# Performance work log

Measured on AMD Instinct MI355X. Metric: run time of the kernel, lower is better.

Reference implementation:

```python
import jax, jax.numpy as jnp
import numpy as np

EPS = 1e-8
N, E = 30000, 480000
SI, VI, SE, VE = 128, 16, 32, 1


def _norm_no_nan(x, axis=-1, keepdims=False, eps=EPS, sqrt=True):
    out = jnp.maximum(jnp.sum(x * x, axis=axis, keepdims=keepdims), eps)
    return jnp.sqrt(out) if sqrt else out


def _gvp(s, v, wh, wsw, wsb, wv, act):
    # v: [n, vi, 3]; wh: [h, vi]; wsw: [so, si+h]; wv: [vo, h]
    vh = jnp.einsum('nct,hc->nht', v, wh)                 # [n, h, 3]
    vn = _norm_no_nan(vh, axis=-1)                        # [n, h]
    s_out = jnp.concatenate([s, vn], -1) @ wsw.T + wsb    # [n, so]
    v_out = jnp.einsum('nht,oh->not', vh, wv)             # [n, vo, 3]
    if act:
        v_out = v_out * jax.nn.sigmoid(_norm_no_nan(v_out, axis=-1, keepdims=True))
        s_out = jax.nn.relu(s_out)
    return s_out, v_out


def _layernorm(s, v, g, b):
    mu = jnp.mean(s, -1, keepdims=True)
    var = jnp.mean((s - mu) ** 2, -1, keepdims=True)
    s = (s - mu) / jnp.sqrt(var + 1e-5) * g + b
    vn = jnp.maximum(jnp.sum(v * v, -1, keepdims=True), EPS)          # [n, vc, 1] squared norms
    mask = (vn > 2 * EPS).astype(v.dtype)
    vm = jnp.sum(vn * mask, -2, keepdims=True) / (EPS + jnp.sum(mask, -2, keepdims=True))
    vm = jnp.sqrt(vm + EPS)
    v = mask * (v / vm)
    return s, v


def setup_inputs() -> dict:
    key = jax.random.key(0)
    ks = iter(jax.random.split(key, 40))

    def p(shape):
        return (jax.random.normal(next(ks), shape, jnp.float32) / np.float32(np.sqrt(shape[-1])))

    inp = {
        's': jax.random.normal(next(ks), (N, SI), jnp.float32),
        'v': jax.random.normal(next(ks), (N, VI, 3), jnp.float32),
        'edge_index': jax.random.randint(next(ks), (2, E), 0, N),
        'edge_s': jax.random.normal(next(ks), (E, SE), jnp.float32),
        'edge_v': jax.random.normal(next(ks), (E, VE, 3), jnp.float32),
    }
    smi, vmi = 2 * SI + SE, 2 * VI + VE      # 288, 33
    h1 = max(vmi, VI)                        # 33
    # message GVP 1: (288,33)->(128,16)
    inp['m1_wh'], inp['m1_wsw'], inp['m1_wsb'], inp['m1_wv'] = p((h1, vmi)), p((SI, smi + h1)), jnp.zeros((SI,), jnp.float32), p((VI, h1))
    # message GVP 2/3: (128,16)->(128,16), h=16
    inp['m2_wh'], inp['m2_wsw'], inp['m2_wsb'], inp['m2_wv'] = p((VI, VI)), p((SI, SI + VI)), jnp.zeros((SI,), jnp.float32), p((VI, VI))
    inp['m3_wh'], inp['m3_wsw'], inp['m3_wsb'], inp['m3_wv'] = p((VI, VI)), p((SI, SI + VI)), jnp.zeros((SI,), jnp.float32), p((VI, VI))
    # feedforward: (128,16)->(512,32)->(128,16)
    sh, vh = 4 * SI, 2 * VI                  # 512, 32
    inp['f1_wh'], inp['f1_wsw'], inp['f1_wsb'], inp['f1_wv'] = p((vh, VI)), p((sh, SI + vh)), jnp.zeros((sh,), jnp.float32), p((vh, vh))
    inp['f2_wh'], inp['f2_wsw'], inp['f2_wsb'], inp['f2_wv'] = p((vh, vh)), p((SI, sh + vh)), jnp.zeros((SI,), jnp.float32), p((VI, vh))
    inp['ln0_g'], inp['ln0_b'] = jnp.ones((SI,), jnp.float32), jnp.zeros((SI,), jnp.float32)
    inp['ln1_g'], inp['ln1_b'] = jnp.ones((SI,), jnp.float32), jnp.zeros((SI,), jnp.float32)
    return inp


def reference(s, v, edge_index, edge_s, edge_v,
              m1_wh, m1_wsw, m1_wsb, m1_wv,
              m2_wh, m2_wsw, m2_wsb, m2_wv,
              m3_wh, m3_wsw, m3_wsb, m3_wv,
              f1_wh, f1_wsw, f1_wsb, f1_wv,
              f2_wh, f2_wsw, f2_wsb, f2_wv,
              ln0_g, ln0_b, ln1_g, ln1_b):
    src, dst = edge_index[0], edge_index[1]
    # gather: tuple_cat((s_j, v_j), edge_attr, (s_i, v_i))
    ms = jnp.concatenate([s[src], edge_s, s[dst]], -1)           # [E, 288]
    mv = jnp.concatenate([v[src], edge_v, v[dst]], -2)           # [E, 33, 3]
    ms, mv = _gvp(ms, mv, m1_wh, m1_wsw, m1_wsb, m1_wv, act=True)
    ms, mv = _gvp(ms, mv, m2_wh, m2_wsw, m2_wsb, m2_wv, act=True)
    ms, mv = _gvp(ms, mv, m3_wh, m3_wsw, m3_wsb, m3_wv, act=False)
    # scatter-mean aggregate to destination nodes
    cnt = jnp.maximum(jax.ops.segment_sum(jnp.ones((mv.shape[0],), ms.dtype), dst, N), 1.0)
    agg_s = jax.ops.segment_sum(ms, dst, N) / cnt[:, None]
    agg_v = jax.ops.segment_sum(mv, dst, N) / cnt[:, None, None]
    # residual + norm (dropout is identity at eval)
    s1, v1 = _layernorm(s + agg_s, v + agg_v, ln0_g, ln0_b)
    # feedforward
    fs, fv = _gvp(s1, v1, f1_wh, f1_wsw, f1_wsb, f1_wv, act=True)
    fs, fv = _gvp(fs, fv, f2_wh, f2_wsw, f2_wsb, f2_wv, act=False)
    s2, v2 = _layernorm(s1 + fs, v1 + fv, ln1_g, ln1_b)
    return s2, v2
```

## Files before the change

kernel.cpp:

```cpp
#include <hip/hip_runtime.h>

#define EPSF 1e-8f

typedef __attribute__((ext_vector_type(8))) short short8;
typedef __attribute__((ext_vector_type(4))) short short4v;
typedef __attribute__((ext_vector_type(4))) float float4v;

__device__ __forceinline__ unsigned bfhi_bits(float x) {
    unsigned u = __float_as_uint(x);
    return (u + 0x7fffu + ((u >> 16) & 1u)) >> 16;
}
__device__ __forceinline__ float bits2f(unsigned b) { return __uint_as_float(b << 16); }
__device__ __forceinline__ void split_bf(float x, unsigned short& h, unsigned short& l) {
    unsigned hb = bfhi_bits(x);
    h = (unsigned short)hb;
    l = (unsigned short)bfhi_bits(x - bits2f(hb));
}

template<int NH>
__device__ __forceinline__ void matvec3_v(const float* __restrict__ wrow,
                                          const float* prow,
                                          float& a0, float& a1, float& a2)
{
    #pragma unroll
    for (int g = 0; g < NH / 4; ++g) {
        const float4 f0 = ((const float4*)prow)[3 * g + 0];
        const float4 f1 = ((const float4*)prow)[3 * g + 1];
        const float4 f2 = ((const float4*)prow)[3 * g + 2];
        const float w0 = wrow[4 * g + 0], w1 = wrow[4 * g + 1];
        const float w2 = wrow[4 * g + 2], w3 = wrow[4 * g + 3];
        a0 = fmaf(w0, f0.x, a0); a1 = fmaf(w0, f0.y, a1); a2 = fmaf(w0, f0.z, a2);
        a0 = fmaf(w1, f0.w, a0); a1 = fmaf(w1, f1.x, a1); a2 = fmaf(w1, f1.y, a2);
        a0 = fmaf(w2, f1.z, a0); a1 = fmaf(w2, f1.w, a1); a2 = fmaf(w2, f2.x, a2);
        a0 = fmaf(w3, f2.y, a0); a1 = fmaf(w3, f2.z, a1); a2 = fmaf(w3, f2.w, a2);
    }
}

__global__ void pack_w(const float* __restrict__ W, unsigned short* __restrict__ hi,
                       unsigned short* __restrict__ lo, int NO, int K, int steps) {
    const int gid = blockIdx.x * 256 + threadIdx.x;
    const int total = (NO >> 4) * steps * 512;
    if (gid >= total) return;
    const int j = gid & 7, l = (gid >> 3) & 63, rest = gid >> 9;
    const int t = rest % steps, nt = rest / steps;
    const int n = nt * 16 + (l & 15);
    const int k = t * 32 + ((l >> 4) << 3) + j;
    const float x = (k < K) ? W[(size_t)n * K + k] : 0.f;
    unsigned short h, lw;
    split_bf(x, h, lw);
    hi[gid] = h; lo[gid] = lw;
}

__global__ void pack_m1e(const float* __restrict__ W, unsigned short* __restrict__ hi,
                         unsigned short* __restrict__ lo) {
    const int gid = blockIdx.x * 256 + threadIdx.x;
    if (gid >= 12288) return;
    const int j = gid & 7, l = (gid >> 3) & 63, rest = gid >> 9;
    const int t = rest % 3, nt = rest / 3;
    const int n = nt * 16 + (l & 15);
    const int k = t * 32 + ((l >> 4) << 3) + j;
    float x = 0.f;
    if (k < 32)      x = W[(size_t)n * 321 + 128 + k];
    else if (k < 65) x = W[(size_t)n * 321 + 288 + (k - 32)];
    unsigned short h, lw; split_bf(x, h, lw);
    hi[gid] = h; lo[gid] = lw;
}

__global__ void pack_m1n(const float* __restrict__ W, unsigned short* __restrict__ hi,
                         unsigned short* __restrict__ lo) {
    const int gid = blockIdx.x * 256 + threadIdx.x;
    if (gid >= 32768) return;
    const int j = gid & 7, l = (gid >> 3) & 63, rest = gid >> 9;
    const int t = rest & 3, nt = rest >> 2;
    const int n = nt * 16 + (l & 15);
    const int k = t * 32 + ((l >> 4) << 3) + j;
    const float x = (n < 128) ? W[(size_t)n * 321 + k]
                              : W[(size_t)(n - 128) * 321 + 160 + k];
    unsigned short h, lw; split_bf(x, h, lw);
    hi[gid] = h; lo[gid] = lw;
}

template<int STEPS, int NTPW, int ASTR, int MCLAMP = 15>
__device__ __forceinline__ void kloop(const unsigned short* PAh, const unsigned short* PAl,
    const unsigned short* __restrict__ wph, const unsigned short* __restrict__ wpl,
    float4v* acc, int lane, int wave)
{
    const int m = (lane & 15) & MCLAMP, q = lane >> 4;
    for (int t = 0; t < STEPS; ++t) {
        const int k0 = t * 32 + q * 8;
        const short8 ah = *(const short8*)(PAh + m * ASTR + k0);
        const short8 al = *(const short8*)(PAl + m * ASTR + k0);
        #pragma unroll
        for (int i = 0; i < NTPW; ++i) {
            const int nt = wave * NTPW + i;
            const size_t off = ((size_t)(nt * STEPS + t) * 64 + lane) * 8;
            const short8 bh = *(const short8*)(wph + off);
            const short8 bl = *(const short8*)(wpl + off);
            acc[i] = __builtin_amdgcn_mfma_f32_16x16x32_bf16(ah, bh, acc[i], 0, 0, 0);
            acc[i] = __builtin_amdgcn_mfma_f32_16x16x32_bf16(al, bh, acc[i], 0, 0, 0);
            acc[i] = __builtin_amdgcn_mfma_f32_16x16x32_bf16(ah, bl, acc[i], 0, 0, 0);
        }
    }
}

constexpr int PAS = 136;

__global__ __launch_bounds__(256)
void node_pre(const float* __restrict__ s, const float* __restrict__ v,
              const float* __restrict__ m1_wh, const float* __restrict__ m1_wsb,
              const unsigned short* __restrict__ pnh, const unsigned short* __restrict__ pnl,
              float* __restrict__ Pg, float* __restrict__ Q1g, float* __restrict__ Q3g,
              int N)
{
    __shared__ __align__(16) unsigned short Ah[16 * PAS], Al[16 * PAS];
    __shared__ __align__(16) float Vs[16 * 48];

    const int tid = threadIdx.x, lane = tid & 63, wave = tid >> 6;
    const int e = tid & 15, q16 = tid >> 4;
    const int n0 = blockIdx.x * 16;
    const int ne = min(n0 + e, N - 1);

    {
        const float* sp = s + (size_t)ne * 128 + q16 * 8;
        const float4 x = ((const float4*)sp)[0];
        const float4 y = ((const float4*)sp)[1];
        short8 hv, lv; unsigned short h, l;
        split_bf(x.x, h, l); hv[0] = h; lv[0] = l;
        split_bf(x.y, h, l); hv[1] = h; lv[1] = l;
        split_bf(x.z, h, l); hv[2] = h; lv[2] = l;
        split_bf(x.w, h, l); hv[3] = h; lv[3] = l;
        split_bf(y.x, h, l); hv[4] = h; lv[4] = l;
        split_bf(y.y, h, l); hv[5] = h; lv[5] = l;
        split_bf(y.z, h, l); hv[6] = h; lv[6] = l;
        split_bf(y.w, h, l); hv[7] = h; lv[7] = l;
        *(short8*)(Ah + e * PAS + q16 * 8) = hv;
        *(short8*)(Al + e * PAS + q16 * 8) = lv;
    }
    if (q16 < 12)
        ((float4*)(Vs + e * 48))[q16] = ((const float4*)(v + (size_t)ne * 48))[q16];
    __syncthreads();

    {
        float4v acc[4] = {{0,0,0,0},{0,0,0,0},{0,0,0,0},{0,0,0,0}};
        kloop<4, 4, PAS>(Ah, Al, pnh, pnl, acc, lane, wave);
        const int q = lane >> 4;
        #pragma unroll
        for (int i = 0; i < 4; ++i) {
            const int j = (wave * 4 + i) * 16 + (lane & 15);
            const float bias = (j < 128) ? m1_wsb[j] : 0.f;
            #pragma unroll
            for (int r = 0; r < 4; ++r) {
                const int m = q * 4 + r;
                if (n0 + m < N) Pg[(size_t)(n0 + m) * 256 + j] = acc[i][r] + bias;
            }
        }
    }
    #pragma unroll
    for (int k = 0; k < 7; ++k) {
        const int idx = tid + k * 256;
        if (idx < 16 * 99) {
            const int n = idx & 15, j = idx >> 4;
            const int h = j / 3, t = j - h * 3;
            const float* vb = Vs + n * 48 + t;
            const float* w = m1_wh + h * 33;
            float a1 = 0.f, a3 = 0.f;
            for (int c = 0; c < 16; ++c) {
                const float vv = vb[c * 3];
                a1 = fmaf(w[c], vv, a1);
                a3 = fmaf(w[17 + c], vv, a3);
            }
            const int nn = n0 + n;
            if (nn < N) {
                Q1g[(size_t)nn * 100 + j] = a1;
                Q3g[(size_t)nn * 100 + j] = a3;
            }
        }
    }
}

constexpr int SA2 = 168;
constexpr int SBs = 168;
constexpr int SB1 = 100;
constexpr int SB2 = 52;
constexpr int SPS = 132;

__global__ __launch_bounds__(256)
void edge_kernel(const int* __restrict__ eidx,
                 const float* __restrict__ es, const float* __restrict__ ev,
                 const float* __restrict__ m1_wh, const float* __restrict__ m1_wv,
                 const float* __restrict__ m2_wh, const float* __restrict__ m2_wsb,
                 const float* __restrict__ m2_wv,
                 const float* __restrict__ m3_wh, const float* __restrict__ m3_wsb,
                 const float* __restrict__ m3_wv,
                 const unsigned short* __restrict__ p1h, const unsigned short* __restrict__ p1l,
                 const unsigned short* __restrict__ p2h, const unsigned short* __restrict__ p2l,
                 const unsigned short* __restrict__ p3h, const unsigned short* __restrict__ p3l,
                 const float* __restrict__ Pg, const float* __restrict__ Q1g,
                 const float* __restrict__ Q3g,
                 double* __restrict__ agg_s, double* __restrict__ agg_v,
                 float* __restrict__ cnt, int E)
{
    __shared__ __align__(16) unsigned short Ah[16 * SA2], Al[16 * SA2];
    __shared__ __align__(16) float SP[16 * SPS];
    __shared__ __align__(16) float B1[16 * SB1];
    __shared__ int ssrc[16], sgd[16], sdst[16], seid[16];

    unsigned short* PBh = Ah;
    unsigned short* PBl = Al;
    float* B2 = SP;

    const int tid = threadIdx.x, lane = tid & 63, wave = tid >> 6;
    const int e = tid & 15, q16 = tid >> 4;
    const int e0 = blockIdx.x * 16;

    const int eg_r = e0 + e;
    const int ee_r = (eg_r < E) ? eg_r : (E - 1);
    const int src_r = eidx[ee_r];
    const int dst_r = eidx[E + ee_r];

    if (q16 < 8) {
        const float4 x = ((const float4*)(es + (size_t)ee_r * 32))[q16];
        short4v hv, lv; unsigned short h, l;
        split_bf(x.x, h, l); hv[0] = h; lv[0] = l;
        split_bf(x.y, h, l); hv[1] = h; lv[1] = l;
        split_bf(x.z, h, l); hv[2] = h; lv[2] = l;
        split_bf(x.w, h, l); hv[3] = h; lv[3] = l;
        *(short4v*)(Ah + e * SA2 + 4 * q16) = hv;
        *(short4v*)(Al + e * SA2 + 4 * q16) = lv;
    }
    { const int c = 65 + q16; Ah[e * SA2 + c] = 0; Al[e * SA2 + c] = 0; }
    { const int c = 81 + q16; if (c < 96) { Ah[e * SA2 + c] = 0; Al[e * SA2 + c] = 0; } }
    {
        const float* P1 = Pg + (size_t)src_r * 256;
        const float* P3 = Pg + (size_t)dst_r * 256 + 128;
        const float4 a0 = ((const float4*)P1)[2 * q16];
        const float4 a1 = ((const float4*)P1)[2 * q16 + 1];
        const float4 b0 = ((const float4*)P3)[2 * q16];
        const float4 b1 = ((const float4*)P3)[2 * q16 + 1];
        float4 r0, r1;
        r0.x = a0.x + b0.x; r0.y = a0.y + b0.y; r0.z = a0.z + b0.z; r0.w = a0.w + b0.w;
        r1.x = a1.x + b1.x; r1.y = a1.y + b1.y; r1.z = a1.z + b1.z; r1.w = a1.w + b1.w;
        float4* o = (float4*)(SP + e * SPS + 8 * q16);
        o[0] = r0; o[1] = r1;
    }
    if (tid < 16) {
        const int eg = e0 + tid;
        const bool ok = (eg < E);
        const int ee = ok ? eg : (E - 1);
        seid[tid] = ee;
        ssrc[tid] = eidx[ee];
        const int d = eidx[E + ee];
        sgd[tid] = d;
        sdst[tid] = ok ? d : -1;
    }
    __syncthreads();

    #pragma unroll
    for (int k = 0; k < 3; ++k) {
        const int idx = tid + k * 256;
        if (idx < 528) {
            const int h = idx >> 4, e2 = idx & 15;
            const float* q1 = Q1g + (size_t)ssrc[e2] * 100 + h * 3;
            const float* q3 = Q3g + (size_t)sgd[e2] * 100 + h * 3;
            const float* evp = ev + (size_t)seid[e2] * 3;
            const float w16 = m1_wh[h * 33 + 16];
            const float v0 = q1[0] + q3[0] + w16 * evp[0];
            const float v1 = q1[1] + q3[1] + w16 * evp[1];
            const float v2 = q1[2] + q3[2] + w16 * evp[2];
            float* o = B1 + e2 * SB1 + h * 3;
            o[0] = v0; o[1] = v1; o[2] = v2;
            const float vn = sqrtf(fmaxf(v0 * v0 + v1 * v1 + v2 * v2, EPSF));
            unsigned short hh, ll; split_bf(vn, hh, ll);
            Ah[e2 * SA2 + 32 + h] = hh; Al[e2 * SA2 + 32 + h] = ll;
        }
    }
    __syncthreads();

    float4v acc1[2] = {{0,0,0,0},{0,0,0,0}};
    kloop<3, 2, SA2>(Ah, Al, p1h, p1l, acc1, lane, wave);
    __syncthreads();

    {
        const int q = lane >> 4;
        #pragma unroll
        for (int i = 0; i < 2; ++i) {
            const int n = (wave * 2 + i) * 16 + (lane & 15);
            #pragma unroll
            for (int r = 0; r < 4; ++r) {
                const int m = q * 4 + r;
                const float x = fmaxf(acc1[i][r] + SP[m * SPS + n], 0.f);
                unsigned short h, l; split_bf(x, h, l);
                PBh[m * SBs + n] = h; PBl[m * SBs + n] = l;
            }
        }
    }
    __syncthreads();

    {
        const int o = q16;
        const float* wrow = m1_wv + o * 33;
        const float* prow = B1 + e * SB1;
        float a0 = 0.f, a1 = 0.f, a2 = 0.f;
        matvec3_v<32>(wrow, prow, a0, a1, a2);
        const float w32 = wrow[32];
        a0 = fmaf(w32, prow[96], a0); a1 = fmaf(w32, prow[97], a1); a2 = fmaf(w32, prow[98], a2);
        const float nrm = sqrtf(fmaxf(a0 * a0 + a1 * a1 + a2 * a2, EPSF));
        const float sg = 1.f / (1.f + __expf(-nrm));
        float* p2 = B2 + e * SB2 + o * 3;
        p2[0] = a0 * sg; p2[1] = a1 * sg; p2[2] = a2 * sg;
    }
    __syncthreads();

    {
        const int h = q16;
        float a0 = 0.f, a1 = 0.f, a2 = 0.f;
        matvec3_v<16>(m2_wh + h * 16, B2 + e * SB2, a0, a1, a2);
        float* o = B1 + e * SB1 + h * 3;
        o[0] = a0; o[1] = a1; o[2] = a2;
        const float vn = sqrtf(fmaxf(a0 * a0 + a1 * a1 + a2 * a2, EPSF));
        unsigned short hh, ll; split_bf(vn, hh, ll);
        PBh[e * SBs + 128 + h] = hh; PBl[e * SBs + 128 + h] = ll;
        PBh[e * SBs + 144 + h] = 0;  PBl[e * SBs + 144 + h] = 0;
    }
    __syncthreads();

    float4v acc2[2] = {{0,0,0,0},{0,0,0,0}};
    kloop<5, 2, SBs>(PBh, PBl, p2h, p2l, acc2, lane, wave);
    __syncthreads();

    {
        const int q = lane >> 4;
        #pragma unroll
        for (int i = 0; i < 2; ++i) {
            const int n = (wave * 2 + i) * 16 + (lane & 15);
            const float bias = m2_wsb[n];
            #pragma unroll
            for (int r = 0; r < 4; ++r) {
                const int m = q * 4 + r;
                const float x = fmaxf(acc2[i][r] + bias, 0.f);
                unsigned short h, l; split_bf(x, h, l);
                Ah[m * SA2 + n] = h; Al[m * SA2 + n] = l;
            }
        }
    }
    {
        const int o = q16;
        float a0 = 0.f, a1 = 0.f, a2 = 0.f;
        matvec3_v<16>(m2_wv + o * 16, B1 + e * SB1, a0, a1, a2);
        const float nrm = sqrtf(fmaxf(a0 * a0 + a1 * a1 + a2 * a2, EPSF));
        const float sg = 1.f / (1.f + __expf(-nrm));
        float* p2 = B2 + e * SB2 + o * 3;
        p2[0] = a0 * sg; p2[1] = a1 * sg; p2[2] = a2 * sg;
    }
    __syncthreads();

    {
        const int h = q16;
        float a0 = 0.f, a1 = 0.f, a2 = 0.f;
        matvec3_v<16>(m3_wh + h * 16, B2 + e * SB2, a0, a1, a2);
        float* o = B1 + e * SB1 + h * 3;
        o[0] = a0; o[1] = a1; o[2] = a2;
        const float vn = sqrtf(fmaxf(a0 * a0 + a1 * a1 + a2 * a2, EPSF));
        unsigned short hh, ll; split_bf(vn, hh, ll);
        Ah[e * SA2 + 128 + h] = hh; Al[e * SA2 + 128 + h] = ll;
        Ah[e * SA2 + 144 + h] = 0;  Al[e * SA2 + 144 + h] = 0;
    }
    __syncthreads();

    float4v acc3[2] = {{0,0,0,0},{0,0,0,0}};
    kloop<5, 2, SA2>(Ah, Al, p3h, p3l, acc3, lane, wave);
    {
        const int o = q16;
        float a0 = 0.f, a1 = 0.f, a2 = 0.f;
        matvec3_v<16>(m3_wv + o * 16, B1 + e * SB1, a0, a1, a2);
        float* p2 = B2 + e * SB2 + o * 3;
        p2[0] = a0; p2[1] = a1; p2[2] = a2;
    }
    __syncthreads();

    {
        const int q = lane >> 4;
        #pragma unroll
        for (int i = 0; i < 2; ++i) {
            const int n = (wave * 2 + i) * 16 + (lane & 15);
            const float bias = m3_wsb[n];
            #pragma unroll
            for (int r = 0; r < 4; ++r) {
                const int m = q * 4 + r;
                const int d = sdst[m];
                if (d >= 0) atomicAdd(&agg_s[(size_t)d * 128 + n], (double)(acc3[i][r] + bias));
            }
        }
    }
    #pragma unroll
    for (int it = 0; it < 3; ++it) {
        const int j = q16 + 16 * it;
        const int d = sdst[e];
        if (d >= 0) atomicAdd(&agg_v[(size_t)d * 48 + j], (double)B2[e * SB2 + j]);
    }
    if (tid < 16 && sdst[tid] >= 0) atomicAdd(&cnt[sdst[tid]], 1.0f);
}

template<int NE, int SSTR, int VSTR>
__device__ __forceinline__ void layer_normT(float* S, float* V,
    const float* __restrict__ g, const float* __restrict__ b, float* red, int lane)
{
    #pragma unroll
    for (int e = 0; e < NE; ++e) {
        float x0 = S[e * SSTR + lane], x1 = S[e * SSTR + 64 + lane];
        float sum = x0 + x1;
        #pragma unroll
        for (int off = 32; off > 0; off >>= 1) sum += __shfl_xor(sum, off, 64);
        const float mu = sum * (1.f / 128.f);
        const float d0 = x0 - mu, d1 = x1 - mu;
        float vs = d0 * d0 + d1 * d1;
        #pragma unroll
        for (int off = 32; off > 0; off >>= 1) vs += __shfl_xor(vs, off, 64);
        const float rstd = rsqrtf(vs * (1.f / 128.f) + 1e-5f);
        S[e * SSTR + lane]      = d0 * rstd * g[lane]      + b[lane];
        S[e * SSTR + 64 + lane] = d1 * rstd * g[lane + 64] + b[lane + 64];

        if (lane < 16) {
            const float a = V[e * VSTR + lane * 3], bb = V[e * VSTR + lane * 3 + 1],
                        cc = V[e * VSTR + lane * 3 + 2];
            const float vn = fmaxf(a * a + bb * bb + cc * cc, EPSF);
            red[lane]      = vn;
            red[16 + lane] = (vn > 2.f * EPSF) ? 1.f : 0.f;
        }
        __syncthreads();
        float sn = 0.f, sm = 0.f;
        #pragma unroll
        for (int i = 0; i < 16; ++i) { sn += red[i] * red[16 + i]; sm += red[16 + i]; }
        const float rvm = rsqrtf(sn / (EPSF + sm) + EPSF);
        if (lane < 48) V[e * VSTR + lane] = red[16 + lane / 3] * V[e * VSTR + lane] * rvm;
        __syncthreads();
    }
}

constexpr int NNS  = 132;
constexpr int NNV  = 52;
constexpr int NNH  = 100;
constexpr int NA1n = 168;
constexpr int NA2n = 552;

__global__ __launch_bounds__(128)
void node_kernel(const float* __restrict__ s, const float* __restrict__ v,
                 const float* __restrict__ f1_wh, const float* __restrict__ f1_wsb,
                 const float* __restrict__ f1_wv,
                 const float* __restrict__ f2_wh, const float* __restrict__ f2_wsb,
                 const float* __restrict__ f2_wv,
                 const float* __restrict__ ln0_g, const float* __restrict__ ln0_b,
                 const float* __restrict__ ln1_g, const float* __restrict__ ln1_b,
                 const unsigned short* __restrict__ pf1h, const unsigned short* __restrict__ pf1l,
                 const unsigned short* __restrict__ pf2h, const unsigned short* __restrict__ pf2l,
                 const double* __restrict__ agg_s, const double* __restrict__ agg_v,
                 const float* __restrict__ cnt,
                 float* __restrict__ out, int N)
{
    __shared__ __align__(16) unsigned short UBh[8 * NA1n], UBl[8 * NA1n];
    __shared__ __align__(16) unsigned short UB2h[8 * NA2n], UB2l[8 * NA2n];
    __shared__ __align__(16) float S1f[8 * NNS];
    __shared__ __align__(16) float V1f[8 * NNV];
    __shared__ __align__(16) float VH[8 * NNH];
    __shared__ __align__(16) float FV[8 * NNH];
    __shared__ float red[2 * 32];

    const int tid = threadIdx.x, lane = tid & 63, wave = tid >> 6;
    const int e = tid & 7, qq = tid >> 3;
    const int n0 = blockIdx.x * 8;

    bool oks[4];
    #pragma unroll
    for (int e4 = 0; e4 < 4; ++e4) {
        const int idx = wave * 4 + e4;
        const int ng = n0 + idx;
        oks[e4] = (ng < N);
        const int n = oks[e4] ? ng : (N - 1);
        const double inv = 1.0 / (double)fmaxf(cnt[n], 1.f);
        if (lane < 32) {
            const float4 a = ((const float4*)(s + (size_t)n * 128))[lane];
            const double2 b0 = ((const double2*)(agg_s + (size_t)n * 128))[2 * lane];
            const double2 b1 = ((const double2*)(agg_s + (size_t)n * 128))[2 * lane + 1];
            float4 r;
            r.x = (float)((double)a.x + b0.x * inv);
            r.y = (float)((double)a.y + b0.y * inv);
            r.z = (float)((double)a.z + b1.x * inv);
            r.w = (float)((double)a.w + b1.y * inv);
            ((float4*)(S1f + idx * NNS))[lane] = r;
        }
        if (lane < 12) {
            const float4 a = ((const float4*)(v + (size_t)n * 48))[lane];
            const double2 b0 = ((const double2*)(agg_v + (size_t)n * 48))[2 * lane];
            const double2 b1 = ((const double2*)(agg_v + (size_t)n * 48))[2 * lane + 1];
            float4 r;
            r.x = (float)((double)a.x + b0.x * inv);
            r.y = (float)((double)a.y + b0.y * inv);
            r.z = (float)((double)a.z + b1.x * inv);
            r.w = (float)((double)a.w + b1.y * inv);
            ((float4*)(V1f + idx * NNV))[lane] = r;
        }
    }
    __syncthreads();

    layer_normT<4, NNS, NNV>(S1f + wave * 4 * NNS, V1f + wave * 4 * NNV,
                             ln0_g, ln0_b, red + wave * 32, lane);

    {
        const float* sp = S1f + e * NNS + qq * 8;
        short8 hv, lv; unsigned short h, l;
        #pragma unroll
        for (int j = 0; j < 8; ++j) { split_bf(sp[j], h, l); hv[j] = h; lv[j] = l; }
        *(short8*)(UBh + e * NA1n + qq * 8) = hv;
        *(short8*)(UBl + e * NA1n + qq * 8) = lv;
    }
    #pragma unroll
    for (int hi = 0; hi < 2; ++hi) {
        const int h = qq + 16 * hi;
        float a0 = 0.f, a1 = 0.f, a2 = 0.f;
        matvec3_v<16>(f1_wh + h * 16, V1f + e * NNV, a0, a1, a2);
        float* o = VH + e * NNH + h * 3;
        o[0] = a0; o[1] = a1; o[2] = a2;
        const float vn = sqrtf(fmaxf(a0 * a0 + a1 * a1 + a2 * a2, EPSF));
        unsigned short hh, ll; split_bf(vn, hh, ll);
        UBh[e * NA1n + 128 + h] = hh; UBl[e * NA1n + 128 + h] = ll;
    }
    __syncthreads();

    {
        float4v acc1[16];
        #pragma unroll
        for (int i = 0; i < 16; ++i) acc1[i] = (float4v){0.f, 0.f, 0.f, 0.f};
        kloop<5, 16, NA1n>(UBh, UBl, pf1h, pf1l, acc1, lane, wave);
        const int q = lane >> 4;
        #pragma unroll
        for (int i = 0; i < 16; ++i) {
            const int n = (wave * 16 + i) * 16 + (lane & 15);
            const float bias = f1_wsb[n];
            #pragma unroll
            for (int r = 0; r < 4; ++r) {
                const int m = q * 4 + r;
                if (m < 8) {
                    const float x = fmaxf(acc1[i][r] + bias, 0.f);
                    unsigned short h, l; split_bf(x, h, l);
                    UB2h[m * NA2n + n] = h; UB2l[m * NA2n + n] = l;
                }
            }
        }
    }
    #pragma unroll
    for (int oi = 0; oi < 2; ++oi) {
        const int o = qq + 16 * oi;
        float a0 = 0.f, a1 = 0.f, a2 = 0.f;
        matvec3_v<32>(f1_wv + o * 32, VH + e * NNH, a0, a1, a2);
        const float nrm = sqrtf(fmaxf(a0 * a0 + a1 * a1 + a2 * a2, EPSF));
        const float sg = 1.f / (1.f + __expf(-nrm));
        float* p2 = FV + e * NNH + o * 3;
        p2[0] = a0 * sg; p2[1] = a1 * sg; p2[2] = a2 * sg;
    }
    __syncthreads();

    #pragma unroll
    for (int hi = 0; hi < 2; ++hi) {
        const int h = qq + 16 * hi;
        float a0 = 0.f, a1 = 0.f, a2 = 0.f;
        matvec3_v<32>(f2_wh + h * 32, FV + e * NNH, a0, a1, a2);
        float* o = VH + e * NNH + h * 3;
        o[0] = a0; o[1] = a1; o[2] = a2;
        const float vn = sqrtf(fmaxf(a0 * a0 + a1 * a1 + a2 * a2, EPSF));
        unsigned short hh, ll; split_bf(vn, hh, ll);
        UB2h[e * NA2n + 512 + h] = hh; UB2l[e * NA2n + 512 + h] = ll;
    }
    __syncthreads();

    {
        float4v acc2[4] = {{0,0,0,0},{0,0,0,0},{0,0,0,0},{0,0,0,0}};
        kloop<17, 4, NA2n, 7>(UB2h, UB2l, pf2h, pf2l, acc2, lane, wave);
        const int q = lane >> 4;
        #pragma unroll
        for (int i = 0; i < 4; ++i) {
            const int n = (wave * 4 + i) * 16 + (lane & 15);
            const float bias = f2_wsb[n];
            #pragma unroll
            for (int r = 0; r < 4; ++r) {
                const int m = q * 4 + r;
                if (m < 8) S1f[m * NNS + n] += acc2[i][r] + bias;
            }
        }
    }
    {
        const int o = qq;
        float a0 = 0.f, a1 = 0.f, a2 = 0.f;
        matvec3_v<32>(f2_wv + o * 32, VH + e * NNH, a0, a1, a2);
        float* p2 = V1f + e * NNV + o * 3;
        p2[0] += a0; p2[1] += a1; p2[2] += a2;
    }
    __syncthreads();

    layer_normT<4, NNS, NNV>(S1f + wave * 4 * NNS, V1f + wave * 4 * NNV,
                             ln1_g, ln1_b, red + wave * 32, lane);

    #pragma unroll
    for (int e4 = 0; e4 < 4; ++e4) {
        if (!oks[e4]) continue;
        const int idx = wave * 4 + e4;
        const int n = n0 + idx;
        if (lane < 32)
            ((float4*)(out + (size_t)n * 128))[lane] = ((const float4*)(S1f + idx * NNS))[lane];
        if (lane < 12)
            ((float4*)(out + (size_t)N * 128 + (size_t)n * 48))[lane] =
                ((const float4*)(V1f + idx * NNV))[lane];
    }
}

extern "C" void kernel_launch(void* const* d_in, const int* in_sizes, int n_in,
                              void* d_out, int out_size, void* d_ws, size_t ws_size,
                              hipStream_t stream)
{
    const float* s    = (const float*)d_in[0];
    const float* v    = (const float*)d_in[1];
    const int*   eidx = (const int*)d_in[2];
    const float* es   = (const float*)d_in[3];
    const float* ev   = (const float*)d_in[4];
    const float* m1_wh = (const float*)d_in[5];
    const float* m1_wsw = (const float*)d_in[6];
    const float* m1_wsb = (const float*)d_in[7];
    const float* m1_wv = (const float*)d_in[8];
    const float* m2_wh = (const float*)d_in[9];
    const float* m2_wsw = (const float*)d_in[10];
    const float* m2_wsb = (const float*)d_in[11];
    const float* m2_wv = (const float*)d_in[12];
    const float* m3_wh = (const float*)d_in[13];
    const float* m3_wsw = (const float*)d_in[14];
    const float* m3_wsb = (const float*)d_in[15];
    const float* m3_wv = (const float*)d_in[16];
    const float* f1_wh = (const float*)d_in[17];
    const float* f1_wsw = (const float*)d_in[18];
    const float* f1_wsb = (const float*)d_in[19];
    const float* f1_wv = (const float*)d_in[20];
    const float* f2_wh = (const float*)d_in[21];
    const float* f2_wsw = (const float*)d_in[22];
    const float* f2_wsb = (const float*)d_in[23];
    const float* f2_wv = (const float*)d_in[24];
    const float* ln0_g = (const float*)d_in[25];
    const float* ln0_b = (const float*)d_in[26];
    const float* ln1_g = (const float*)d_in[27];
    const float* ln1_b = (const float*)d_in[28];

    const int N = in_sizes[0] / 128;
    const int E = in_sizes[2] / 2;

    double* agg_s = (double*)d_ws;
    double* agg_v = agg_s + (size_t)N * 128;
    float* cnt    = (float*)(agg_v + (size_t)N * 48);
    unsigned short* pk =
        (unsigned short*)(((uintptr_t)(cnt + N) + 15) & ~(uintptr_t)15);
    const int S_P1E = 12288, S_M23 = 20480, S_MN = 32768, S_F1 = 81920, S_F2 = 69632;
    unsigned short* p1h = pk;            unsigned short* p1l = p1h + S_P1E;
    unsigned short* p2h = p1l + S_P1E;   unsigned short* p2l = p2h + S_M23;
    unsigned short* p3h = p2l + S_M23;   unsigned short* p3l = p3h + S_M23;
    unsigned short* pnh = p3l + S_M23;   unsigned short* pnl = pnh + S_MN;
    unsigned short* pf1h = pnl + S_MN;   unsigned short* pf1l = pf1h + S_F1;
    unsigned short* pf2h = pf1l + S_F1;  unsigned short* pf2l = pf2h + S_F2;
    float* Pg  = (float*)(((uintptr_t)(pf2l + S_F2) + 15) & ~(uintptr_t)15);
    float* Q1g = Pg + (size_t)N * 256;
    float* Q3g = Q1g + (size_t)N * 100;

    hipMemsetAsync(d_ws, 0,
                   (size_t)N * 176 * sizeof(double) + (size_t)N * sizeof(float),
                   stream);

    pack_m1e<<<dim3((12288 + 255) / 256), dim3(256), 0, stream>>>(m1_wsw, p1h, p1l);
    pack_w<<<dim3((S_M23 + 255) / 256), dim3(256), 0, stream>>>(m2_wsw, p2h, p2l, 128, 144, 5);
    pack_w<<<dim3((S_M23 + 255) / 256), dim3(256), 0, stream>>>(m3_wsw, p3h, p3l, 128, 144, 5);
    pack_m1n<<<dim3((32768 + 255) / 256), dim3(256), 0, stream>>>(m1_wsw, pnh, pnl);
    pack_w<<<dim3((S_F1 + 255) / 256), dim3(256), 0, stream>>>(f1_wsw, pf1h, pf1l, 512, 160, 5);
    pack_w<<<dim3((S_F2 + 255) / 256), dim3(256), 0, stream>>>(f2_wsw, pf2h, pf2l, 128, 544, 17);

    node_pre<<<dim3((N + 15) / 16), dim3(256), 0, stream>>>(
        s, v, m1_wh, m1_wsb, pnh, pnl, Pg, Q1g, Q3g, N);

    edge_kernel<<<dim3((E + 15) / 16), dim3(256), 0, stream>>>(
        eidx, es, ev,
        m1_wh, m1_wv,
        m2_wh, m2_wsb, m2_wv,
        m3_wh, m3_wsb, m3_wv,
        p1h, p1l, p2h, p2l, p3h, p3l,
        Pg, Q1g, Q3g,
        agg_s, agg_v, cnt, E);

    node_kernel<<<dim3((N + 7) / 8), dim3(128), 0, stream>>>(
        s, v,
        f1_wh, f1_wsb, f1_wv,
        f2_wh, f2_wsb, f2_wv,
        ln0_g, ln0_b, ln1_g, ln1_b,
        pf1h, pf1l, pf2h, pf2l,
        agg_s, agg_v, cnt,
        (float*)d_out, N);
}
```

Before: 1.247 ms.

## Run edge kernel as single-wave blocks processing eight edges each

Shrinks the edge kernel from 256-thread blocks handling 16 edges to 64-thread, single-wave blocks handling 8 edges. The one wave now covers all 128 output columns of each matrix product, with 8 accumulator tiles per lane, and the per-thread vector loops iterate to cover the missing threads. The aim is cheaper barriers and more independent blocks for latency hiding. In exchange, half of each 16-row MFMA tile is wasted on padding rows, packed weights are fetched twice as often per edge, and each lane holds more registers.

```diff
diff --git a/kernel.cpp b/kernel.cpp
--- a/kernel.cpp
+++ b/kernel.cpp
@@ -184,7 +184,7 @@
 constexpr int SB2 = 52;
 constexpr int SPS = 132;
 
-__global__ __launch_bounds__(256)
+__global__ __launch_bounds__(64)
 void edge_kernel(const int* __restrict__ eidx,
                  const float* __restrict__ es, const float* __restrict__ ev,
                  const float* __restrict__ m1_wh, const float* __restrict__ m1_wv,
@@ -200,66 +200,67 @@
                  double* __restrict__ agg_s, double* __restrict__ agg_v,
                  float* __restrict__ cnt, int E)
 {
-    __shared__ __align__(16) unsigned short Ah[16 * SA2], Al[16 * SA2];
-    __shared__ __align__(16) float SP[16 * SPS];
-    __shared__ __align__(16) float B1[16 * SB1];
-    __shared__ int ssrc[16], sgd[16], sdst[16], seid[16];
+    __shared__ __align__(16) unsigned short Ah[8 * SA2], Al[8 * SA2];
+    __shared__ __align__(16) float SP[8 * SPS];
+    __shared__ __align__(16) float B1[8 * SB1];
+    __shared__ int ssrc[8], sgd[8], sdst[8], seid[8];
 
     unsigned short* PBh = Ah;
     unsigned short* PBl = Al;
     float* B2 = SP;
 
-    const int tid = threadIdx.x, lane = tid & 63, wave = tid >> 6;
-    const int e = tid & 15, q16 = tid >> 4;
-    const int e0 = blockIdx.x * 16;
+    const int lane = threadIdx.x & 63;
+    const int e = lane & 7, q8 = lane >> 3;
+    const int e0 = blockIdx.x * 8;
 
     const int eg_r = e0 + e;
     const int ee_r = (eg_r < E) ? eg_r : (E - 1);
     const int src_r = eidx[ee_r];
     const int dst_r = eidx[E + ee_r];
 
-    if (q16 < 8) {
-        const float4 x = ((const float4*)(es + (size_t)ee_r * 32))[q16];
+    {
+        const float4 x = ((const float4*)(es + (size_t)ee_r * 32))[q8];
         short4v hv, lv; unsigned short h, l;
         split_bf(x.x, h, l); hv[0] = h; lv[0] = l;
         split_bf(x.y, h, l); hv[1] = h; lv[1] = l;
         split_bf(x.z, h, l); hv[2] = h; lv[2] = l;
         split_bf(x.w, h, l); hv[3] = h; lv[3] = l;
-        *(short4v*)(Ah + e * SA2 + 4 * q16) = hv;
-        *(short4v*)(Al + e * SA2 + 4 * q16) = lv;
-    }
-    { const int c = 65 + q16; Ah[e * SA2 + c] = 0; Al[e * SA2 + c] = 0; }
-    { const int c = 81 + q16; if (c < 96) { Ah[e * SA2 + c] = 0; Al[e * SA2 + c] = 0; } }
+        *(short4v*)(Ah + e * SA2 + 4 * q8) = hv;
+        *(short4v*)(Al + e * SA2 + 4 * q8) = lv;
+    }
+    { const int c = 65 + q8; Ah[e * SA2 + c] = 0; Al[e * SA2 + c] = 0; }
+    { const int c = 73 + q8; Ah[e * SA2 + c] = 0; Al[e * SA2 + c] = 0; }
+    { const int c = 81 + q8; Ah[e * SA2 + c] = 0; Al[e * SA2 + c] = 0; }
+    { const int c = 89 + q8; if (c < 96) { Ah[e * SA2 + c] = 0; Al[e * SA2 + c] = 0; } }
     {
         const float* P1 = Pg + (size_t)src_r * 256;
         const float* P3 = Pg + (size_t)dst_r * 256 + 128;
-        const float4 a0 = ((const float4*)P1)[2 * q16];
-        const float4 a1 = ((const float4*)P1)[2 * q16 + 1];
-        const float4 b0 = ((const float4*)P3)[2 * q16];
-        const float4 b1 = ((const float4*)P3)[2 * q16 + 1];
-        float4 r0, r1;
-        r0.x = a0.x + b0.x; r0.y = a0.y + b0.y; r0.z = a0.z + b0.z; r0.w = a0.w + b0.w;
-        r1.x = a1.x + b1.x; r1.y = a1.y + b1.y; r1.z = a1.z + b1.z; r1.w = a1.w + b1.w;
-        float4* o = (float4*)(SP + e * SPS + 8 * q16);
-        o[0] = r0; o[1] = r1;
-    }
-    if (tid < 16) {
-        const int eg = e0 + tid;
+        #pragma unroll
+        for (int j = 0; j < 4; ++j) {
+            const float4 a = ((const float4*)P1)[4 * q8 + j];
+            const float4 b = ((const float4*)P3)[4 * q8 + j];
+            float4 r;
+            r.x = a.x + b.x; r.y = a.y + b.y; r.z = a.z + b.z; r.w = a.w + b.w;
+            ((float4*)(SP + e * SPS + 16 * q8))[j] = r;
+        }
+    }
+    if (lane < 8) {
+        const int eg = e0 + lane;
         const bool ok = (eg < E);
         const int ee = ok ? eg : (E - 1);
-        seid[tid] = ee;
-        ssrc[tid] = eidx[ee];
+        seid[lane] = ee;
+        ssrc[lane] = eidx[ee];
         const int d = eidx[E + ee];
-        sgd[tid] = d;
-        sdst[tid] = ok ? d : -1;
-    }
-    __syncthreads();
-
-    #pragma unroll
-    for (int k = 0; k < 3; ++k) {
-        const int idx = tid + k * 256;
-        if (idx < 528) {
-            const int h = idx >> 4, e2 = idx & 15;
+        sgd[lane] = d;
+        sdst[lane] = ok ? d : -1;
+    }
+    __syncthreads();
+
+    #pragma unroll
+    for (int k = 0; k < 5; ++k) {
+        const int idx = lane + k * 64;
+        if (idx < 264) {
+            const int h = idx >> 3, e2 = idx & 7;
             const float* q1 = Q1g + (size_t)ssrc[e2] * 100 + h * 3;
             const float* q3 = Q3g + (size_t)sgd[e2] * 100 + h * 3;
             const float* evp = ev + (size_t)seid[e2] * 3;
@@ -276,28 +277,33 @@
     }
     __syncthreads();
 
-    float4v acc1[2] = {{0,0,0,0},{0,0,0,0}};
-    kloop<3, 2, SA2>(Ah, Al, p1h, p1l, acc1, lane, wave);
+    float4v acc1[8];
+    #pragma unroll
+    for (int i = 0; i < 8; ++i) acc1[i] = (float4v){0.f, 0.f, 0.f, 0.f};
+    kloop<3, 8, SA2, 7>(Ah, Al, p1h, p1l, acc1, lane, 0);
     __syncthreads();
 
     {
         const int q = lane >> 4;
         #pragma unroll
-        for (int i = 0; i < 2; ++i) {
-            const int n = (wave * 2 + i) * 16 + (lane & 15);
+        for (int i = 0; i < 8; ++i) {
+            const int n = i * 16 + (lane & 15);
             #pragma unroll
             for (int r = 0; r < 4; ++r) {
                 const int m = q * 4 + r;
-                const float x = fmaxf(acc1[i][r] + SP[m * SPS + n], 0.f);
-                unsigned short h, l; split_bf(x, h, l);
-                PBh[m * SBs + n] = h; PBl[m * SBs + n] = l;
+                if (m < 8) {
+                    const float x = fmaxf(acc1[i][r] + SP[m * SPS + n], 0.f);
+                    unsigned short h, l; split_bf(x, h, l);
+                    PBh[m * SBs + n] = h; PBl[m * SBs + n] = l;
+                }
             }
         }
     }
     __syncthreads();
 
-    {
-        const int o = q16;
+    #pragma unroll
+    for (int it = 0; it < 2; ++it) {
+        const int o = q8 + 8 * it;
         const float* wrow = m1_wv + o * 33;
         const float* prow = B1 + e * SB1;
         float a0 = 0.f, a1 = 0.f, a2 = 0.f;
@@ -311,8 +317,9 @@
     }
     __syncthreads();
 
-    {
-        const int h = q16;
+    #pragma unroll
+    for (int it = 0; it < 2; ++it) {
+        const int h = q8 + 8 * it;
         float a0 = 0.f, a1 = 0.f, a2 = 0.f;
         matvec3_v<16>(m2_wh + h * 16, B2 + e * SB2, a0, a1, a2);
         float* o = B1 + e * SB1 + h * 3;
@@ -324,27 +331,33 @@
     }
     __syncthreads();
 
-    float4v acc2[2] = {{0,0,0,0},{0,0,0,0}};
-    kloop<5, 2, SBs>(PBh, PBl, p2h, p2l, acc2, lane, wave);
+    float4v acc2[8];
+    #pragma unroll
+    for (int i = 0; i < 8; ++i) acc2[i] = (float4v){0.f, 0.f, 0.f, 0.f};
+    kloop<5, 8, SBs, 7>(PBh, PBl, p2h, p2l, acc2, lane, 0);
     __syncthreads();
 
     {
         const int q = lane >> 4;
         #pragma unroll
-        for (int i = 0; i < 2; ++i) {
-            const int n = (wave * 2 + i) * 16 + (lane & 15);
+        for (int i = 0; i < 8; ++i) {
+            const int n = i * 16 + (lane & 15);
             const float bias = m2_wsb[n];
             #pragma unroll
             for (int r = 0; r < 4; ++r) {
                 const int m = q * 4 + r;
-                const float x = fmaxf(acc2[i][r] + bias, 0.f);
-                unsigned short h, l; split_bf(x, h, l);
-                Ah[m * SA2 + n] = h; Al[m * SA2 + n] = l;
+                if (m < 8) {
+                    const float x = fmaxf(acc2[i][r] + bias, 0.f);
+                    unsigned short h, l; split_bf(x, h, l);
+                    Ah[m * SA2 + n] = h; Al[m * SA2 + n] = l;
+                }
             }
         }
     }
-    {
-        const int o = q16;
+    __syncthreads();
+    #pragma unroll
+    for (int it = 0; it < 2; ++it) {
+        const int o = q8 + 8 * it;
         float a0 = 0.f, a1 = 0.f, a2 = 0.f;
         matvec3_v<16>(m2_wv + o * 16, B1 + e * SB1, a0, a1, a2);
         const float nrm = sqrtf(fmaxf(a0 * a0 + a1 * a1 + a2 * a2, EPSF));
@@ -354,8 +367,9 @@
     }
     __syncthreads();
 
-    {
-        const int h = q16;
+    #pragma unroll
+    for (int it = 0; it < 2; ++it) {
+        const int h = q8 + 8 * it;
         float a0 = 0.f, a1 = 0.f, a2 = 0.f;
         matvec3_v<16>(m3_wh + h * 16, B2 + e * SB2, a0, a1, a2);
         float* o = B1 + e * SB1 + h * 3;
@@ -367,10 +381,13 @@
     }
     __syncthreads();
 
-    float4v acc3[2] = {{0,0,0,0},{0,0,0,0}};
-    kloop<5, 2, SA2>(Ah, Al, p3h, p3l, acc3, lane, wave);
-    {
-        const int o = q16;
+    float4v acc3[8];
+    #pragma unroll
+    for (int i = 0; i < 8; ++i) acc3[i] = (float4v){0.f, 0.f, 0.f, 0.f};
+    kloop<5, 8, SA2, 7>(Ah, Al, p3h, p3l, acc3, lane, 0);
+    #pragma unroll
+    for (int it = 0; it < 2; ++it) {
+        const int o = q8 + 8 * it;
         float a0 = 0.f, a1 = 0.f, a2 = 0.f;
         matvec3_v<16>(m3_wv + o * 16, B1 + e * SB1, a0, a1, a2);
         float* p2 = B2 + e * SB2 + o * 3;
@@ -381,24 +398,26 @@
     {
         const int q = lane >> 4;
         #pragma unroll
-        for (int i = 0; i < 2; ++i) {
-            const int n = (wave * 2 + i) * 16 + (lane & 15);
+        for (int i = 0; i < 8; ++i) {
+            const int n = i * 16 + (lane & 15);
             const float bias = m3_wsb[n];
             #pragma unroll
             for (int r = 0; r < 4; ++r) {
                 const int m = q * 4 + r;
-                const int d = sdst[m];
-                if (d >= 0) atomicAdd(&agg_s[(size_t)d * 128 + n], (double)(acc3[i][r] + bias));
+                if (m < 8) {
+                    const int d = sdst[m];
+                    if (d >= 0) atomicAdd(&agg_s[(size_t)d * 128 + n], (double)(acc3[i][r] + bias));
+                }
             }
         }
     }
     #pragma unroll
-    for (int it = 0; it < 3; ++it) {
-        const int j = q16 + 16 * it;
+    for (int it = 0; it < 6; ++it) {
+        const int j = q8 + 8 * it;
         const int d = sdst[e];
         if (d >= 0) atomicAdd(&agg_v[(size_t)d * 48 + j], (double)B2[e * SB2 + j]);
     }
-    if (tid < 16 && sdst[tid] >= 0) atomicAdd(&cnt[sdst[tid]], 1.0f);
+    if (lane < 8 && sdst[lane] >= 0) atomicAdd(&cnt[sdst[lane]], 1.0f);
 }
 
 template<int NE, int SSTR, int VSTR>
@@ -679,7 +698,7 @@
     node_pre<<<dim3((N + 15) / 16), dim3(256), 0, stream>>>(
         s, v, m1_wh, m1_wsb, pnh, pnl, Pg, Q1g, Q3g, N);
 
-    edge_kernel<<<dim3((E + 15) / 16), dim3(256), 0, stream>>>(
+    edge_kernel<<<dim3((E + 7) / 8), dim3(64), 0, stream>>>(
         eidx, es, ev,
         m1_wh, m1_wv,
         m2_wh, m2_wsb, m2_wv,
```

Measured after the change: 1.983 ms. 1.59x slower.
